# Kernel tuning notes

Measured on AMD Instinct MI355X. Metric: run time of the kernel, lower is better.

The kernel has to match this reference:

```python
import jax, jax.numpy as jnp
import numpy as np

CANVAS_SIZE = 224
N_SEGMENTS = 4
N_SAMPLES = 50
SOFTNESS = 0.02


def setup_inputs() -> dict:
    key = jax.random.key(0)
    k1, k2 = jax.random.split(key)
    n_paths = 1024
    paths_control_points = jax.random.uniform(k1, (n_paths, N_SEGMENTS, 4, 2), dtype=jnp.float32)
    colors = jax.random.uniform(k2, (n_paths, 4), dtype=jnp.float32)
    return {"paths_control_points": paths_control_points, "colors": colors}


def reference(paths_control_points, colors):
    H = W = CANVAS_SIZE
    n_paths = paths_control_points.shape[0]

    # Cubic Bezier basis at t in linspace(0,1,50)[:-1]  -> (49, 4)
    t = jnp.linspace(0.0, 1.0, N_SAMPLES)[:-1]
    mt = 1.0 - t
    basis = jnp.stack([mt**3, 3.0 * mt**2 * t, 3.0 * mt * t**2, t**3], axis=-1)

    # Sample all curve points for all paths/segments at once: (P, S, T, 2)
    pts = jnp.einsum('tc,psce->pste', basis, paths_control_points)
    pts = pts.reshape(n_paths, -1, 2)  # (P, S*T, 2) == (P, 196, 2)

    center = pts.mean(axis=1)  # (P, 2) -> (x, y)
    avg_radius = jnp.linalg.norm(pts - center[:, None, :], axis=-1).mean(axis=1)  # (P,)

    # Pixel grid in [0,1], 'ij' indexing: grid_y varies over rows, grid_x over cols
    lin = jnp.linspace(0.0, 1.0, H)
    grid_y, grid_x = jnp.meshgrid(lin, lin, indexing='ij')  # (H, W) each

    # Distance field per path: (P, H, W)
    dx = grid_x[None] - center[:, 0, None, None]
    dy = grid_y[None] - center[:, 1, None, None]
    dist = jnp.sqrt(dx * dx + dy * dy)

    # Soft disk mask scaled by per-path alpha: (P, H, W)
    masks = jax.nn.sigmoid((avg_radius[:, None, None] - dist) / SOFTNESS)
    masks = masks * colors[:, 3, None, None]

    # Sequential front-to-back alpha compositing (order matters) via scan
    canvas0 = jnp.ones((3, H, W), dtype=paths_control_points.dtype)

    def step(canvas, xs):
        m, c = xs  # m: (H, W), c: (3,)
        canvas = canvas * (1.0 - m)[None] + c[:, None, None] * m[None]
        return canvas, None

    canvas, _ = jax.lax.scan(step, canvas0, (masks, colors[:, :3]))
    return canvas
```

## Files before the change

### kernel.cpp

```cpp
#include <hip/hip_runtime.h>
#include <math.h>

#define NPATHS   1024
#define CANVAS_H 224
#define CANVAS_W 224
#define NPIX     (CANVAS_H * CANVAS_W)
#define NSAMP    49
#define K2EXP    72.134752f
#define CULL_MARGIN 0.3f

#define NWAVES   8
#define PPW      (NPATHS / NWAVES)


__global__ __launch_bounds__(256) void path_setup_kernel(
    const float* __restrict__ cps,
    const float* __restrict__ colors,
    float* __restrict__ pd)
{
    const int tid = blockIdx.x * 256 + threadIdx.x;
    const int p = tid >> 2;
    const int s = tid & 3;

    const float4* cp4 = reinterpret_cast<const float4*>(cps);
    float4 a = cp4[p * 8 + s * 2];
    float4 b = cp4[p * 8 + s * 2 + 1];

    float sx = 0.0f, sy = 0.0f;
    for (int i = 0; i < NSAMP; ++i) {
        float t  = (float)i * (1.0f / 49.0f);
        float mt = 1.0f - t;
        float b0 = mt * mt * mt;
        float b1 = 3.0f * mt * mt * t;
        float b2 = 3.0f * mt * t * t;
        float b3 = t * t * t;
        sx += b0 * a.x + b1 * a.z + b2 * b.x + b3 * b.z;
        sy += b0 * a.y + b1 * a.w + b2 * b.y + b3 * b.w;
    }
    sx += __shfl_xor(sx, 1); sx += __shfl_xor(sx, 2);
    sy += __shfl_xor(sy, 1); sy += __shfl_xor(sy, 2);
    const float inv_n = 1.0f / 196.0f;
    float cx = sx * inv_n;
    float cy = sy * inv_n;

    float sr = 0.0f;
    for (int i = 0; i < NSAMP; ++i) {
        float t  = (float)i * (1.0f / 49.0f);
        float mt = 1.0f - t;
        float b0 = mt * mt * mt;
        float b1 = 3.0f * mt * mt * t;
        float b2 = 3.0f * mt * t * t;
        float b3 = t * t * t;
        float ptx = b0 * a.x + b1 * a.z + b2 * b.x + b3 * b.z;
        float pty = b0 * a.y + b1 * a.w + b2 * b.y + b3 * b.w;
        float dx = ptx - cx;
        float dy = pty - cy;
        sr += sqrtf(dx * dx + dy * dy);
    }
    sr += __shfl_xor(sr, 1); sr += __shfl_xor(sr, 2);
    float r = sr * inv_n;

    if (s == 0) {
        float4 col = reinterpret_cast<const float4*>(colors)[p];
        float rc = r + CULL_MARGIN;
        float4* o = reinterpret_cast<float4*>(pd) + (size_t)p * 2;
        o[0] = make_float4(cx, cy, -K2EXP * r, col.w);
        o[1] = make_float4(col.x * col.w, col.y * col.w, col.z * col.w, rc * rc);
    }
}

__global__ __launch_bounds__(512) void render_kernel(
    const float* __restrict__ pd,
    float* __restrict__ out)
{
    __shared__ float4 xch[NWAVES * 64];

    const int wave = threadIdx.x >> 6;
    const int lane = threadIdx.x & 63;
    const int lx = lane & 7;
    const int ly = lane >> 3;
    const int xx = blockIdx.x * 8 + lx;
    const int yy = blockIdx.y * 8 + ly;
    const float px = (float)xx * (1.0f / 223.0f);
    const float py = (float)yy * (1.0f / 223.0f);

    const float4* __restrict__ pdv = reinterpret_cast<const float4*>(pd);
    const int base = __builtin_amdgcn_readfirstlane(wave * (PPW * 2));

    float T = 1.0f, Ar = 0.0f, Ag = 0.0f, Ab = 0.0f;

#pragma unroll 4
    for (int p = 0; p < PPW; ++p) {
        float4 d0 = pdv[base + 2 * p];
        float4 d1 = pdv[base + 2 * p + 1];
        float dx = px - d0.x;
        float dy = py - d0.y;
        float d2 = __builtin_fmaf(dx, dx, dy * dy);
        if (__any(d2 < d1.w)) {
            float dist = __builtin_amdgcn_sqrtf(d2);
            float e = __builtin_amdgcn_exp2f(__builtin_fmaf(dist, K2EXP, d0.z));
            float q = __builtin_amdgcn_rcpf(1.0f + e);
            float om = __builtin_fmaf(-d0.w, q, 1.0f);
            T  = T * om;
            Ar = __builtin_fmaf(Ar, om, d1.x * q);
            Ag = __builtin_fmaf(Ag, om, d1.y * q);
            Ab = __builtin_fmaf(Ab, om, d1.z * q);
        }
    }

    xch[wave * 64 + lane] = make_float4(T, Ar, Ag, Ab);
    __syncthreads();

    if (wave == 0) {
        float R = 1.0f, G = 1.0f, B = 1.0f;
#pragma unroll
        for (int w = 0; w < NWAVES; ++w) {
            float4 c = xch[w * 64 + lane];
            R = __builtin_fmaf(R, c.x, c.y);
            G = __builtin_fmaf(G, c.x, c.z);
            B = __builtin_fmaf(B, c.x, c.w);
        }
        const int pix = yy * CANVAS_W + xx;
        out[pix]            = R;
        out[NPIX + pix]     = G;
        out[2 * NPIX + pix] = B;
    }
}

extern "C" void kernel_launch(void* const* d_in, const int* in_sizes, int n_in,
                              void* d_out, int out_size, void* d_ws, size_t ws_size,
                              hipStream_t stream) {
    const float* cps    = (const float*)d_in[0];
    const float* colors = (const float*)d_in[1];
    float* out = (float*)d_out;
    float* pd  = (float*)d_ws;

    path_setup_kernel<<<(NPATHS * 4) / 256, 256, 0, stream>>>(cps, colors, pd);

    dim3 grid(CANVAS_W / 8, CANVAS_H / 8);
    render_kernel<<<grid, 512, 0, stream>>>(pd, out);
}
```

Before: 45.70 us.

## Render two pixels per lane with scalar-loaded double-buffered path data, drop culling

Each lane now computes two pixels (rows y and y+4) that share the same dx, so the block covers 16x8 pixels and the grid is halved. Path parameters are fetched into scalar registers with inline s_load_dwordx16, double-buffered so the next batch loads while the current one is processed. The red/green accumulation uses two-wide float vectors so it can map to packed FMA. The per-path wave-level culling test is removed and every path is now evaluated for every pixel, which adds transcendental work but removes the branch and the vote.

```diff
diff --git a/kernel.cpp b/kernel.cpp
--- a/kernel.cpp
+++ b/kernel.cpp
@@ -7,11 +7,15 @@
 #define NPIX     (CANVAS_H * CANVAS_W)
 #define NSAMP    49
 #define K2EXP    72.134752f
-#define CULL_MARGIN 0.3f
 
 #define NWAVES   8
 #define PPW      (NPATHS / NWAVES)
 
+
+typedef __attribute__((ext_vector_type(16))) int   i16x16;
+typedef __attribute__((ext_vector_type(2)))  float f32x2;
+
+__device__ __forceinline__ float sf(int v) { return __int_as_float(v); }
 
 __global__ __launch_bounds__(256) void path_setup_kernel(
     const float* __restrict__ cps,
@@ -62,10 +66,9 @@
 
     if (s == 0) {
         float4 col = reinterpret_cast<const float4*>(colors)[p];
-        float rc = r + CULL_MARGIN;
         float4* o = reinterpret_cast<float4*>(pd) + (size_t)p * 2;
         o[0] = make_float4(cx, cy, -K2EXP * r, col.w);
-        o[1] = make_float4(col.x * col.w, col.y * col.w, col.z * col.w, rc * rc);
+        o[1] = make_float4(col.x * col.w, col.y * col.w, col.z * col.w, 0.0f);
     }
 }
 
@@ -73,57 +76,101 @@
     const float* __restrict__ pd,
     float* __restrict__ out)
 {
-    __shared__ float4 xch[NWAVES * 64];
+    __shared__ float4 xch[NWAVES * 2 * 64];
 
-    const int wave = threadIdx.x >> 6;
+    const int wave = __builtin_amdgcn_readfirstlane((int)(threadIdx.x >> 6));
     const int lane = threadIdx.x & 63;
-    const int lx = lane & 7;
-    const int ly = lane >> 3;
-    const int xx = blockIdx.x * 8 + lx;
-    const int yy = blockIdx.y * 8 + ly;
-    const float px = (float)xx * (1.0f / 223.0f);
-    const float py = (float)yy * (1.0f / 223.0f);
+    const int lx = lane & 15;
+    const int lq = lane >> 4;
+    const int xx  = blockIdx.x * 16 + lx;
+    const int yy0 = blockIdx.y * 8 + lq;
+    const float px  = (float)xx  * (1.0f / 223.0f);
+    const float py0 = (float)yy0 * (1.0f / 223.0f);
+    const float py1 = (float)(yy0 + 4) * (1.0f / 223.0f);
 
-    const float4* __restrict__ pdv = reinterpret_cast<const float4*>(pd);
-    const int base = __builtin_amdgcn_readfirstlane(wave * (PPW * 2));
+    const float* wptr = pd + (size_t)wave * (PPW * 8);
 
-    float T = 1.0f, Ar = 0.0f, Ag = 0.0f, Ab = 0.0f;
+    float T0 = 1.0f, Ab0 = 0.0f, T1 = 1.0f, Ab1 = 0.0f;
+    f32x2 ra0; ra0.x = 0.0f; ra0.y = 0.0f;
+    f32x2 ra1; ra1.x = 0.0f; ra1.y = 0.0f;
 
-#pragma unroll 4
-    for (int p = 0; p < PPW; ++p) {
-        float4 d0 = pdv[base + 2 * p];
-        float4 d1 = pdv[base + 2 * p + 1];
-        float dx = px - d0.x;
-        float dy = py - d0.y;
-        float d2 = __builtin_fmaf(dx, dx, dy * dy);
-        if (__any(d2 < d1.w)) {
-            float dist = __builtin_amdgcn_sqrtf(d2);
-            float e = __builtin_amdgcn_exp2f(__builtin_fmaf(dist, K2EXP, d0.z));
-            float q = __builtin_amdgcn_rcpf(1.0f + e);
-            float om = __builtin_fmaf(-d0.w, q, 1.0f);
-            T  = T * om;
-            Ar = __builtin_fmaf(Ar, om, d1.x * q);
-            Ag = __builtin_fmaf(Ag, om, d1.y * q);
-            Ab = __builtin_fmaf(Ab, om, d1.z * q);
-        }
+#define PBODY(blk, o)                                                        \
+    {                                                                        \
+        float cx  = sf(blk[(o) + 0]);                                        \
+        float cy  = sf(blk[(o) + 1]);                                        \
+        float c2  = sf(blk[(o) + 2]);                                        \
+        float al  = sf(blk[(o) + 3]);                                        \
+        float crx = sf(blk[(o) + 4]);                                        \
+        float cgy = sf(blk[(o) + 5]);                                        \
+        float cba = sf(blk[(o) + 6]);                                        \
+        float dx  = px - cx;                                                 \
+        float dx2 = dx * dx;                                                 \
+        float dy0 = py0 - cy;                                                \
+        float dy1 = py1 - cy;                                                \
+        float d20 = __builtin_fmaf(dy0, dy0, dx2);                           \
+        float d21 = __builtin_fmaf(dy1, dy1, dx2);                           \
+        float s0 = __builtin_amdgcn_sqrtf(d20);                              \
+        float s1 = __builtin_amdgcn_sqrtf(d21);                              \
+        float e0 = __builtin_amdgcn_exp2f(__builtin_fmaf(s0, K2EXP, c2));    \
+        float e1 = __builtin_amdgcn_exp2f(__builtin_fmaf(s1, K2EXP, c2));    \
+        float q0 = __builtin_amdgcn_rcpf(1.0f + e0);                         \
+        float q1 = __builtin_amdgcn_rcpf(1.0f + e1);                         \
+        float om0 = __builtin_fmaf(-al, q0, 1.0f);                           \
+        float om1 = __builtin_fmaf(-al, q1, 1.0f);                           \
+        f32x2 crg; crg.x = crx; crg.y = cgy;                                 \
+        f32x2 om0v; om0v.x = om0; om0v.y = om0;                              \
+        f32x2 om1v; om1v.x = om1; om1v.y = om1;                              \
+        f32x2 q0v;  q0v.x = q0;  q0v.y = q0;                                 \
+        f32x2 q1v;  q1v.x = q1;  q1v.y = q1;                                 \
+        ra0 = ra0 * om0v + crg * q0v;                                        \
+        ra1 = ra1 * om1v + crg * q1v;                                        \
+        T0 *= om0;                                                           \
+        T1 *= om1;                                                           \
+        Ab0 = __builtin_fmaf(Ab0, om0, cba * q0);                            \
+        Ab1 = __builtin_fmaf(Ab1, om1, cba * q1);                            \
     }
 
-    xch[wave * 64 + lane] = make_float4(T, Ar, Ag, Ab);
+    i16x16 A0, A1, B0, B1;
+    asm volatile("s_load_dwordx16 %0, %1, 0x0" : "=s"(A0) : "s"(wptr));
+    asm volatile("s_load_dwordx16 %0, %1, 0x0" : "=s"(A1) : "s"(wptr + 16));
+    asm volatile("s_waitcnt lgkmcnt(0)" : "+s"(A0), "+s"(A1));
+
+    for (int i = 0; i < PPW / 8; ++i) {
+        const float* gB = wptr + (size_t)(i * 64 + 32);
+        asm volatile("s_load_dwordx16 %0, %1, 0x0" : "=s"(B0) : "s"(gB));
+        asm volatile("s_load_dwordx16 %0, %1, 0x0" : "=s"(B1) : "s"(gB + 16));
+        PBODY(A0, 0) PBODY(A0, 8) PBODY(A1, 0) PBODY(A1, 8)
+        asm volatile("s_waitcnt lgkmcnt(0)" : "+s"(B0), "+s"(B1));
+        if (i < PPW / 8 - 1) {
+            const float* gA = wptr + (size_t)(i * 64 + 64);
+            asm volatile("s_load_dwordx16 %0, %1, 0x0" : "=s"(A0) : "s"(gA));
+            asm volatile("s_load_dwordx16 %0, %1, 0x0" : "=s"(A1) : "s"(gA + 16));
+        }
+        PBODY(B0, 0) PBODY(B0, 8) PBODY(B1, 0) PBODY(B1, 8)
+        asm volatile("s_waitcnt lgkmcnt(0)" : "+s"(A0), "+s"(A1));
+    }
+#undef PBODY
+
+    xch[wave * 128 + lane]      = make_float4(T0, ra0.x, ra0.y, Ab0);
+    xch[wave * 128 + 64 + lane] = make_float4(T1, ra1.x, ra1.y, Ab1);
     __syncthreads();
 
     if (wave == 0) {
-        float R = 1.0f, G = 1.0f, B = 1.0f;
 #pragma unroll
-        for (int w = 0; w < NWAVES; ++w) {
-            float4 c = xch[w * 64 + lane];
-            R = __builtin_fmaf(R, c.x, c.y);
-            G = __builtin_fmaf(G, c.x, c.z);
-            B = __builtin_fmaf(B, c.x, c.w);
+        for (int sub = 0; sub < 2; ++sub) {
+            float R = 1.0f, G = 1.0f, Bb = 1.0f;
+#pragma unroll
+            for (int w = 0; w < NWAVES; ++w) {
+                float4 c = xch[w * 128 + sub * 64 + lane];
+                R  = __builtin_fmaf(R,  c.x, c.y);
+                G  = __builtin_fmaf(G,  c.x, c.z);
+                Bb = __builtin_fmaf(Bb, c.x, c.w);
+            }
+            const int pix = (yy0 + sub * 4) * CANVAS_W + xx;
+            out[pix]            = R;
+            out[NPIX + pix]     = G;
+            out[2 * NPIX + pix] = Bb;
         }
-        const int pix = yy * CANVAS_W + xx;
-        out[pix]            = R;
-        out[NPIX + pix]     = G;
-        out[2 * NPIX + pix] = B;
     }
 }
 
@@ -137,6 +184,6 @@
 
     path_setup_kernel<<<(NPATHS * 4) / 256, 256, 0, stream>>>(cps, colors, pd);
 
-    dim3 grid(CANVAS_W / 8, CANVAS_H / 8);
+    dim3 grid(CANVAS_W / 16, CANVAS_H / 8);
     render_kernel<<<grid, 512, 0, stream>>>(pd, out);
 }
```

Result: no change. 44.97 us (-1.6%).

## Stage path data in LDS, compute two pixels per thread, drop culling

Applied to the files above, without the earlier changes.

The render kernel now loads all per-path data into shared memory once per block instead of reading it from global memory in every wave. Each thread handles two pixels rows apart, so each path load and dx computation is reused, and the block grows to 16 waves of 1024 threads. Path centers are pre-scaled by the exponent constant to save a multiply. The wave-uniform bounding-circle cull is removed and every path is evaluated unconditionally, which trades skipped work for branch-free code. The setup kernel now uses 64-thread blocks.

```diff
diff --git a/kernel.cpp b/kernel.cpp
--- a/kernel.cpp
+++ b/kernel.cpp
@@ -7,18 +7,19 @@
 #define NPIX     (CANVAS_H * CANVAS_W)
 #define NSAMP    49
 #define K2EXP    72.134752f
-#define CULL_MARGIN 0.3f
 
-#define NWAVES   8
+#define NWAVES   16
 #define PPW      (NPATHS / NWAVES)
 
 
-__global__ __launch_bounds__(256) void path_setup_kernel(
+__device__ __forceinline__ float sf(int v) { return __int_as_float(v); }
+
+__global__ __launch_bounds__(64) void path_setup_kernel(
     const float* __restrict__ cps,
     const float* __restrict__ colors,
     float* __restrict__ pd)
 {
-    const int tid = blockIdx.x * 256 + threadIdx.x;
+    const int tid = blockIdx.x * 64 + threadIdx.x;
     const int p = tid >> 2;
     const int s = tid & 3;
 
@@ -62,68 +63,89 @@
 
     if (s == 0) {
         float4 col = reinterpret_cast<const float4*>(colors)[p];
-        float rc = r + CULL_MARGIN;
         float4* o = reinterpret_cast<float4*>(pd) + (size_t)p * 2;
-        o[0] = make_float4(cx, cy, -K2EXP * r, col.w);
-        o[1] = make_float4(col.x * col.w, col.y * col.w, col.z * col.w, rc * rc);
+        o[0] = make_float4(cx * K2EXP, cy * K2EXP, -K2EXP * r, col.w);
+        o[1] = make_float4(col.x * col.w, col.y * col.w, col.z * col.w, 0.0f);
     }
 }
 
-__global__ __launch_bounds__(512) void render_kernel(
+__global__ __launch_bounds__(1024) void render_kernel(
     const float* __restrict__ pd,
     float* __restrict__ out)
 {
-    __shared__ float4 xch[NWAVES * 64];
+    __shared__ float4 lds[NPATHS * 2];
 
-    const int wave = threadIdx.x >> 6;
+    {
+        const float4* src = reinterpret_cast<const float4*>(pd);
+        lds[threadIdx.x]        = src[threadIdx.x];
+        lds[threadIdx.x + 1024] = src[threadIdx.x + 1024];
+    }
+    __syncthreads();
+
+    const int wave = __builtin_amdgcn_readfirstlane((int)(threadIdx.x >> 6));
     const int lane = threadIdx.x & 63;
-    const int lx = lane & 7;
-    const int ly = lane >> 3;
-    const int xx = blockIdx.x * 8 + lx;
-    const int yy = blockIdx.y * 8 + ly;
-    const float px = (float)xx * (1.0f / 223.0f);
-    const float py = (float)yy * (1.0f / 223.0f);
+    const int lx = lane & 15;
+    const int lq = lane >> 4;
+    const int xx  = blockIdx.x * 16 + lx;
+    const int yy0 = blockIdx.y * 8 + lq;
+    const float pxs  = (float)xx * (K2EXP / 223.0f);
+    const float py0s = (float)yy0 * (K2EXP / 223.0f);
+    const float py1s = (float)(yy0 + 4) * (K2EXP / 223.0f);
 
-    const float4* __restrict__ pdv = reinterpret_cast<const float4*>(pd);
-    const int base = __builtin_amdgcn_readfirstlane(wave * (PPW * 2));
+    const float4* plds = lds + wave * (PPW * 2);
 
-    float T = 1.0f, Ar = 0.0f, Ag = 0.0f, Ab = 0.0f;
+    float T0 = 1.0f, Ar0 = 0.0f, Ag0 = 0.0f, Ab0 = 0.0f;
+    float T1 = 1.0f, Ar1 = 0.0f, Ag1 = 0.0f, Ab1 = 0.0f;
 
 #pragma unroll 4
     for (int p = 0; p < PPW; ++p) {
-        float4 d0 = pdv[base + 2 * p];
-        float4 d1 = pdv[base + 2 * p + 1];
-        float dx = px - d0.x;
-        float dy = py - d0.y;
-        float d2 = __builtin_fmaf(dx, dx, dy * dy);
-        if (__any(d2 < d1.w)) {
-            float dist = __builtin_amdgcn_sqrtf(d2);
-            float e = __builtin_amdgcn_exp2f(__builtin_fmaf(dist, K2EXP, d0.z));
-            float q = __builtin_amdgcn_rcpf(1.0f + e);
-            float om = __builtin_fmaf(-d0.w, q, 1.0f);
-            T  = T * om;
-            Ar = __builtin_fmaf(Ar, om, d1.x * q);
-            Ag = __builtin_fmaf(Ag, om, d1.y * q);
-            Ab = __builtin_fmaf(Ab, om, d1.z * q);
-        }
+        float4 d0 = plds[2 * p];
+        float4 d1 = plds[2 * p + 1];
+        float dx  = pxs - d0.x;
+        float dy0 = py0s - d0.y;
+        float dy1 = py1s - d0.y;
+        float dx2 = dx * dx;
+        float d20 = __builtin_fmaf(dy0, dy0, dx2);
+        float d21 = __builtin_fmaf(dy1, dy1, dx2);
+        float s0 = __builtin_amdgcn_sqrtf(d20);
+        float s1 = __builtin_amdgcn_sqrtf(d21);
+        float e0 = __builtin_amdgcn_exp2f(s0 + d0.z);
+        float e1 = __builtin_amdgcn_exp2f(s1 + d0.z);
+        float q0 = __builtin_amdgcn_rcpf(1.0f + e0);
+        float q1 = __builtin_amdgcn_rcpf(1.0f + e1);
+        float om0 = __builtin_fmaf(-d0.w, q0, 1.0f);
+        float om1 = __builtin_fmaf(-d0.w, q1, 1.0f);
+        T0 *= om0;
+        T1 *= om1;
+        Ar0 = __builtin_fmaf(Ar0, om0, d1.x * q0);
+        Ag0 = __builtin_fmaf(Ag0, om0, d1.y * q0);
+        Ab0 = __builtin_fmaf(Ab0, om0, d1.z * q0);
+        Ar1 = __builtin_fmaf(Ar1, om1, d1.x * q1);
+        Ag1 = __builtin_fmaf(Ag1, om1, d1.y * q1);
+        Ab1 = __builtin_fmaf(Ab1, om1, d1.z * q1);
     }
 
-    xch[wave * 64 + lane] = make_float4(T, Ar, Ag, Ab);
+    __syncthreads();
+    lds[wave * 128 + lane]      = make_float4(T0, Ar0, Ag0, Ab0);
+    lds[wave * 128 + 64 + lane] = make_float4(T1, Ar1, Ag1, Ab1);
     __syncthreads();
 
     if (wave == 0) {
-        float R = 1.0f, G = 1.0f, B = 1.0f;
 #pragma unroll
-        for (int w = 0; w < NWAVES; ++w) {
-            float4 c = xch[w * 64 + lane];
-            R = __builtin_fmaf(R, c.x, c.y);
-            G = __builtin_fmaf(G, c.x, c.z);
-            B = __builtin_fmaf(B, c.x, c.w);
+        for (int sub = 0; sub < 2; ++sub) {
+            float R = 1.0f, G = 1.0f, Bb = 1.0f;
+#pragma unroll
+            for (int w = 0; w < NWAVES; ++w) {
+                float4 c = lds[w * 128 + sub * 64 + lane];
+                R  = __builtin_fmaf(R,  c.x, c.y);
+                G  = __builtin_fmaf(G,  c.x, c.z);
+                Bb = __builtin_fmaf(Bb, c.x, c.w);
+            }
+            const int pix = (yy0 + sub * 4) * CANVAS_W + xx;
+            out[pix]            = R;
+            out[NPIX + pix]     = G;
+            out[2 * NPIX + pix] = Bb;
         }
-        const int pix = yy * CANVAS_W + xx;
-        out[pix]            = R;
-        out[NPIX + pix]     = G;
-        out[2 * NPIX + pix] = B;
     }
 }
 
@@ -135,8 +157,8 @@
     float* out = (float*)d_out;
     float* pd  = (float*)d_ws;
 
-    path_setup_kernel<<<(NPATHS * 4) / 256, 256, 0, stream>>>(cps, colors, pd);
+    path_setup_kernel<<<(NPATHS * 4) / 64, 64, 0, stream>>>(cps, colors, pd);
 
-    dim3 grid(CANVAS_W / 8, CANVAS_H / 8);
-    render_kernel<<<grid, 512, 0, stream>>>(pd, out);
+    dim3 grid(CANVAS_W / 16, CANVAS_H / 8);
+    render_kernel<<<grid, 1024, 0, stream>>>(pd, out);
 }
```

After: 44.38 us. 1.03x faster.
